# Kernel optimization log

Measured on AMD Instinct MI355X. Metric: run time of the kernel, lower is better.

The kernel has to match this reference:

```python
import jax, jax.numpy as jnp
import numpy as np

B, N, E, H = 4, 2048, 288, 8
D = E // H  # head_dim = 36


def setup_inputs() -> dict:
    key = jax.random.key(0)
    ks = jax.random.split(key, 8)
    s = 1.0 / np.sqrt(E)
    return {
        "query": jax.random.normal(ks[0], (B, N, E), jnp.float32),
        "key": jax.random.normal(ks[1], (B, N, E), jnp.float32),
        "value": jax.random.normal(ks[2], (B, N, E), jnp.float32),
        "Wq": jax.random.normal(ks[3], (E, E), jnp.float32) * s,
        "bq": jnp.zeros((E,), jnp.float32),
        "Wk": jax.random.normal(ks[4], (E, E), jnp.float32) * s,
        "bk": jnp.zeros((E,), jnp.float32),
        "Wv": jax.random.normal(ks[5], (E, E), jnp.float32) * s,
        "bv": jnp.zeros((E,), jnp.float32),
        "Wo": jax.random.normal(ks[6], (E, E), jnp.float32) * s,
        "bo": jnp.zeros((E,), jnp.float32),
    }


def reference(query, key, value, Wq, bq, Wk, bk, Wv, bv, Wo, bo):
    scaling = float(D) ** (-0.5)
    q = (query @ Wq + bq) * scaling            # (B, N, E), pre-scaled as in source
    k = key @ Wk + bk                          # (B, N, E)
    v = value @ Wv + bv                        # (B, N, E)
    # split heads: per-head slices along last dim == reshape to (B, N, H, D)
    qh = q.reshape(B, N, H, D)
    kh = k.reshape(B, N, H, D)
    vh = v.reshape(B, N, H, D)
    scores = jnp.einsum("bnhd,bmhd->bhnm", qh, kh)   # (B, H, N, N)
    attn = jax.nn.softmax(scores, axis=-1)
    out = jnp.einsum("bhnm,bmhd->bnhd", attn, vh)    # (B, N, H, D)
    out = out.reshape(B, N, E)                       # concat heads
    return out @ Wo + bo
```

## Files before the change

kernel.cpp:

```cpp
#include <hip/hip_runtime.h>

#define E 288
#define NSEQ 2048
#define BATCH 4
#define NH 8
#define HD 36
#define BH (BATCH * NH)
#define ROWS (BATCH * NSEQ)
#define BHN (BH * NSEQ)

typedef _Float16 half8_t __attribute__((ext_vector_type(8)));
typedef _Float16 half4_t __attribute__((ext_vector_type(4)));
typedef float f32x4 __attribute__((ext_vector_type(4)));
typedef int i32x4 __attribute__((ext_vector_type(4)));

__device__ __forceinline__ int sw64(int row, int col) {
  return (row << 6) + ((((col >> 3) ^ row) & 7) << 3) + (col & 7);
}

__device__ __forceinline__ int toff(int r, int k) {
  const int rp = r >> 1;
  const int g = (((r & 1) << 2) + (k >> 3)) ^ (rp & 7);
  return (rp << 6) + ((g & 7) << 3) + (k & 7);
}

__device__ __forceinline__ void gld16(const _Float16* g, _Float16* l) {
  __builtin_amdgcn_global_load_lds(
      (const __attribute__((address_space(1))) void*)g,
      (__attribute__((address_space(3))) void*)l, 16, 0, 0);
}

__device__ __forceinline__ float fexp2(float x) {
  return __builtin_amdgcn_exp2f(x);
}

#define WBLK 1296
#define QZBLK 2048

__global__ __launch_bounds__(256) void prep_kernel(
    const float* __restrict__ Wq, const float* __restrict__ Wk,
    const float* __restrict__ Wv, const float* __restrict__ Wo,
    _Float16* __restrict__ wblk, _Float16* __restrict__ q16) {
  const int bid = blockIdx.x;
  const int tid = threadIdx.x;
  if (bid < WBLK) {
    const int j = bid * 256 + tid;
    const int m = j / (E * E);
    const int rem = j - m * (E * E);
    const int k = rem / E, n = rem - k * E;
    const float* W = (m == 0) ? Wq : (m == 1) ? Wk : (m == 2) ? Wv : Wo;
    wblk[(size_t)((m * 3 + n / 96) * 9 + (k >> 5)) * 3072 +
         toff(n % 96, k & 31)] = (_Float16)W[(size_t)k * E + n];
  } else {
    const int j = (bid - WBLK) * 256 + tid;
    ((i32x4*)q16)[j] = (i32x4){0, 0, 0, 0};
  }
}

#define PM 128
#define PN 96

struct QKVArgs {
  const float* x[3];
  const float* bias[3];
  _Float16* out[3];
};

__global__ __launch_bounds__(256, 4) void proj_qkv_kernel(
    QKVArgs A, const _Float16* __restrict__ wblk) {
  __shared__ __align__(16) _Float16 abuf[2][4096];
  __shared__ __align__(16) _Float16 wbuf[2][3072];

  const int tid = threadIdx.x;
  const int lane = tid & 63, w = tid >> 6;
  const int quad = lane >> 4, l15 = lane & 15;
  const int mode = blockIdx.z;
  const int RB = blockIdx.x, CT = blockIdx.y;
  const float* __restrict__ x = A.x[mode];
  const _Float16* __restrict__ wb = wblk + (size_t)(mode * 3 + CT) * 9 * 3072;
  const int row0 = RB * PM;

  float4 apre[4];
  auto loadA = [&](int C) {
#pragma unroll
    for (int iu = 0; iu < 4; ++iu) {
      const int i = tid + 256 * iu, r = i >> 3, c4 = i & 7;
      apre[iu] = *(const float4*)&x[(size_t)(row0 + r) * E + C * 32 + c4 * 4];
    }
  };
  auto writeA = [&](_Float16* dst) {
#pragma unroll
    for (int iu = 0; iu < 4; ++iu) {
      const int i = tid + 256 * iu, r = i >> 3, c4 = i & 7;
      half4_t h = {(_Float16)apre[iu].x, (_Float16)apre[iu].y,
                   (_Float16)apre[iu].z, (_Float16)apre[iu].w};
      *(half4_t*)&dst[toff(r, c4 * 4)] = h;
    }
  };

  f32x4 acc[2][6];
#pragma unroll
  for (int t = 0; t < 2; ++t)
#pragma unroll
    for (int nt = 0; nt < 6; ++nt) acc[t][nt] = (f32x4){0.f, 0.f, 0.f, 0.f};

  loadA(0);
  writeA(abuf[0]);
  for (int seg = w; seg < 6; seg += 4)
    gld16(wb + seg * 512 + lane * 8, wbuf[0] + seg * 512);
  loadA(1);

  for (int C = 0; C < 9; ++C) {
    const int cur = C & 1;
    __syncthreads();
    if (C + 1 < 9) {
      for (int seg = w; seg < 6; seg += 4)
        gld16(wb + (C + 1) * 3072 + seg * 512 + lane * 8,
              wbuf[cur ^ 1] + seg * 512);
      writeA(abuf[cur ^ 1]);
      if (C + 2 < 9) loadA(C + 2);
    }
    half8_t ah[2];
#pragma unroll
    for (int t = 0; t < 2; ++t)
      ah[t] = *(const half8_t*)&abuf[cur][toff(w * 32 + t * 16 + l15, quad * 8)];
#pragma unroll
    for (int nt = 0; nt < 6; ++nt) {
      const half8_t bf = *(const half8_t*)&wbuf[cur][toff(nt * 16 + l15, quad * 8)];
#pragma unroll
      for (int t = 0; t < 2; ++t)
        acc[t][nt] = __builtin_amdgcn_mfma_f32_16x16x32_f16(ah[t], bf, acc[t][nt], 0, 0, 0);
    }
  }

  const float* __restrict__ bias = A.bias[mode];
  _Float16* __restrict__ outp = A.out[mode];
  const float scale = (mode == 0) ? 0.24044917348149868f : 1.0f;
  const int col0 = CT * PN;
#pragma unroll
  for (int nt = 0; nt < 6; ++nt) {
    const int col = col0 + nt * 16 + l15;
    const int h = col / 36, d = col - h * 36;
    const float bc = bias[col];
#pragma unroll
    for (int t = 0; t < 2; ++t) {
#pragma unroll
      for (int r = 0; r < 4; ++r) {
        const int row = row0 + w * 32 + t * 16 + quad * 4 + r;
        const int b = row >> 11, n = row & (NSEQ - 1);
        const int bh = b * NH + h;
        const _Float16 val = (_Float16)((acc[t][nt][r] + bc) * scale);
        if (mode == 0) {
          outp[((size_t)bh * NSEQ + n) * 64 + d] = val;
        } else {
          const int kt = n >> 6, c = n & 63;
          if (mode == 1) {
            outp[((size_t)bh * 32 + kt) * 4096 + sw64(c, d)] = val;
          } else {
            const int pc = ((c & 15) << 2) | (c >> 4);
            outp[((size_t)bh * 32 + kt) * 3072 + sw64(d, pc)] = val;
          }
        }
      }
    }
  }
}

#define QB 128
#define KT 64
#define SPLIT 4

__device__ __forceinline__ void stage_tile(const _Float16* kg, const _Float16* vg,
                                           _Float16* kb, _Float16* vb, int w,
                                           int lane) {
#pragma unroll
  for (int seg = w; seg < 8; seg += 4)
    gld16(kg + seg * 512 + lane * 8, kb + seg * 512);
  for (int seg = w; seg < 6; seg += 4)
    gld16(vg + seg * 512 + lane * 8, vb + seg * 512);
}

__global__ __launch_bounds__(256, 4) void attn_kernel(
    const _Float16* __restrict__ q16, const _Float16* __restrict__ kblk,
    const _Float16* __restrict__ vblk, _Float16* __restrict__ pacc16,
    float* __restrict__ psum) {
  __shared__ __align__(16) _Float16 kbuf[2][KT * 64];
  __shared__ __align__(16) _Float16 vbuf[2][48 * 64];
  __shared__ __align__(16) _Float16 pbuf[4][16 * 64];

  const int tid = threadIdx.x;
  const int lane = tid & 63;
  const int w = tid >> 6;
  const int quad = lane >> 4;
  const int l15 = lane & 15;

  const int id = blockIdx.x;
  const int xcd = id & 7;
  const int qb = (id >> 3) & 15;
  const int g = id >> 7;
  const int bhc = g * 8 + xcd;
  const int bh = bhc >> 2;
  const int chunk = bhc & 3;
  const int q0 = qb * QB;

  const _Float16* qbase = q16 + ((size_t)bh * NSEQ + q0 + w * 32) * 64;
  half8_t qf[2][2];
#pragma unroll
  for (int t = 0; t < 2; ++t)
#pragma unroll
    for (int kc = 0; kc < 2; ++kc)
      qf[t][kc] = *(const half8_t*)&qbase[(t * 16 + l15) * 64 + kc * 32 + quad * 8];

  f32x4 oacc[2][3];
#pragma unroll
  for (int t = 0; t < 2; ++t)
#pragma unroll
    for (int nt = 0; nt < 3; ++nt) oacc[t][nt] = (f32x4){0.f, 0.f, 0.f, 0.f};
  float ssum[2][4] = {{0.f, 0.f, 0.f, 0.f}, {0.f, 0.f, 0.f, 0.f}};

  const int t0 = chunk * 8;
  const _Float16* kbase = kblk + ((size_t)bh * 32 + t0) * 4096;
  const _Float16* vbase = vblk + ((size_t)bh * 32 + t0) * 3072;

  stage_tile(kbase, vbase, kbuf[0], vbuf[0], w, lane);

  for (int it = 0; it < 8; ++it) {
    const int cur = it & 1;
    __syncthreads();
    if (it + 1 < 8)
      stage_tile(kbase + (it + 1) * 4096, vbase + (it + 1) * 3072,
                 kbuf[cur ^ 1], vbuf[cur ^ 1], w, lane);

    half8_t vf[2][3];
#pragma unroll
    for (int kc = 0; kc < 2; ++kc)
#pragma unroll
      for (int nt = 0; nt < 3; ++nt)
        vf[kc][nt] = *(const half8_t*)&vbuf[cur][sw64(nt * 16 + l15, kc * 32 + quad * 8)];

#pragma unroll
    for (int t = 0; t < 2; ++t) {
      f32x4 sc[4];
#pragma unroll
      for (int s = 0; s < 4; ++s) {
        const half8_t kf0 = *(const half8_t*)&kbuf[cur][sw64(s * 16 + l15, quad * 8)];
        const half8_t kf1 = *(const half8_t*)&kbuf[cur][sw64(s * 16 + l15, 32 + quad * 8)];
        f32x4 c0 = __builtin_amdgcn_mfma_f32_16x16x32_f16(
            qf[t][0], kf0, (f32x4){0.f, 0.f, 0.f, 0.f}, 0, 0, 0);
        sc[s] = __builtin_amdgcn_mfma_f32_16x16x32_f16(qf[t][1], kf1, c0, 0, 0, 0);
      }
#pragma unroll
      for (int r = 0; r < 4; ++r) {
        const float p0 = fexp2(sc[0][r]);
        const float p1 = fexp2(sc[1][r]);
        const float p2 = fexp2(sc[2][r]);
        const float p3 = fexp2(sc[3][r]);
        ssum[t][r] += (p0 + p1) + (p2 + p3);
        half4_t ph = {(_Float16)p0, (_Float16)p1, (_Float16)p2, (_Float16)p3};
        *(half4_t*)&pbuf[w][sw64(quad * 4 + r, l15 * 4)] = ph;
      }
#pragma unroll
      for (int kc = 0; kc < 2; ++kc) {
        const half8_t af = *(const half8_t*)&pbuf[w][sw64(l15, kc * 32 + quad * 8)];
#pragma unroll
        for (int nt = 0; nt < 3; ++nt)
          oacc[t][nt] = __builtin_amdgcn_mfma_f32_16x16x32_f16(af, vf[kc][nt], oacc[t][nt], 0, 0, 0);
      }
    }
  }

#pragma unroll
  for (int t = 0; t < 2; ++t) {
#pragma unroll
    for (int r = 0; r < 4; ++r) {
      float s = ssum[t][r];
      s += __shfl_xor(s, 1);
      s += __shfl_xor(s, 2);
      s += __shfl_xor(s, 4);
      s += __shfl_xor(s, 8);
      const int row = q0 + w * 32 + t * 16 + quad * 4 + r;
      const size_t gr = (size_t)chunk * BHN + (size_t)bh * NSEQ + row;
      if (l15 == 0) psum[gr] = s;
#pragma unroll
      for (int nt = 0; nt < 3; ++nt) {
        const int col = nt * 16 + l15;
        if (col < HD) pacc16[gr * HD + col] = (_Float16)oacc[t][nt][r];
      }
    }
  }
}

__global__ __launch_bounds__(256) void combine_kernel(
    const _Float16* __restrict__ pacc16, const float* __restrict__ psum,
    _Float16* __restrict__ abh, _Float16* __restrict__ abl) {
  const int idx = blockIdx.x * 256 + threadIdx.x;
  if (idx >= BHN * 9) return;
  const int gr = idx / 9;
  const int d4 = idx - gr * 9;

  float a[4] = {0.f, 0.f, 0.f, 0.f};
  float s = 0.f;
#pragma unroll
  for (int c = 0; c < SPLIT; ++c) {
    const half4_t p = *(const half4_t*)&pacc16[((size_t)c * BHN + gr) * HD + d4 * 4];
#pragma unroll
    for (int j = 0; j < 4; ++j) a[j] += (float)p[j];
    s += psum[(size_t)c * BHN + gr];
  }
  const float inv = 1.0f / s;
  const int bh = gr >> 11;
  const int n = gr & (NSEQ - 1);
  const int b = bh >> 3, h = bh & 7;
  const int row = b * NSEQ + n;
  const int col = h * 36 + d4 * 4;

  half4_t hv, lv;
#pragma unroll
  for (int j = 0; j < 4; ++j) {
    const float val = a[j] * inv;
    const _Float16 hi = (_Float16)val;
    hv[j] = hi;
    lv[j] = (_Float16)(val - (float)hi);
  }
  const size_t o = (size_t)((row >> 6) * 9 + (col >> 5)) * 2048 + toff(row & 63, col & 31);
  *(half4_t*)&abh[o] = hv;
  *(half4_t*)&abl[o] = lv;
}

__global__ __launch_bounds__(256, 4) void proj_o_kernel(
    const _Float16* __restrict__ abh, const _Float16* __restrict__ abl,
    const _Float16* __restrict__ wblk_o, const float* __restrict__ bias,
    float* __restrict__ out) {
  __shared__ __align__(16) _Float16 hbuf[2][2048];
  __shared__ __align__(16) _Float16 lbuf[2][2048];
  __shared__ __align__(16) _Float16 wbuf[2][3072];

  const int tid = threadIdx.x;
  const int lane = tid & 63, w = tid >> 6;
  const int quad = lane >> 4, l15 = lane & 15;
  const int RB = blockIdx.x, CT = blockIdx.y;
  const _Float16* __restrict__ hblk = abh + (size_t)RB * 9 * 2048;
  const _Float16* __restrict__ lblk = abl + (size_t)RB * 9 * 2048;
  const _Float16* __restrict__ wb = wblk_o + (size_t)CT * 9 * 3072;

  f32x4 acc[6];
#pragma unroll
  for (int nt = 0; nt < 6; ++nt) acc[nt] = (f32x4){0.f, 0.f, 0.f, 0.f};

  gld16(hblk + w * 512 + lane * 8, hbuf[0] + w * 512);
  gld16(lblk + w * 512 + lane * 8, lbuf[0] + w * 512);
  for (int seg = w; seg < 6; seg += 4)
    gld16(wb + seg * 512 + lane * 8, wbuf[0] + seg * 512);

  for (int C = 0; C < 9; ++C) {
    const int cur = C & 1;
    __syncthreads();
    if (C + 1 < 9) {
      gld16(hblk + (C + 1) * 2048 + w * 512 + lane * 8, hbuf[cur ^ 1] + w * 512);
      gld16(lblk + (C + 1) * 2048 + w * 512 + lane * 8, lbuf[cur ^ 1] + w * 512);
      for (int seg = w; seg < 6; seg += 4)
        gld16(wb + (C + 1) * 3072 + seg * 512 + lane * 8, wbuf[cur ^ 1] + seg * 512);
    }
    const half8_t ah = *(const half8_t*)&hbuf[cur][toff(w * 16 + l15, quad * 8)];
    const half8_t al = *(const half8_t*)&lbuf[cur][toff(w * 16 + l15, quad * 8)];
#pragma unroll
    for (int nt = 0; nt < 6; ++nt) {
      const half8_t bf = *(const half8_t*)&wbuf[cur][toff(nt * 16 + l15, quad * 8)];
      acc[nt] = __builtin_amdgcn_mfma_f32_16x16x32_f16(ah, bf, acc[nt], 0, 0, 0);
      acc[nt] = __builtin_amdgcn_mfma_f32_16x16x32_f16(al, bf, acc[nt], 0, 0, 0);
    }
  }

#pragma unroll
  for (int nt = 0; nt < 6; ++nt) {
    const int col = CT * PN + nt * 16 + l15;
    const float bc = bias[col];
#pragma unroll
    for (int r = 0; r < 4; ++r) {
      const int row = RB * 64 + w * 16 + quad * 4 + r;
      out[(size_t)row * E + col] = acc[nt][r] + bc;
    }
  }
}

extern "C" void kernel_launch(void* const* d_in, const int* in_sizes, int n_in,
                              void* d_out, int out_size, void* d_ws,
                              size_t ws_size, hipStream_t stream) {
  const float* query = (const float*)d_in[0];
  const float* key_ = (const float*)d_in[1];
  const float* value = (const float*)d_in[2];
  const float* Wq = (const float*)d_in[3];
  const float* bq = (const float*)d_in[4];
  const float* Wk = (const float*)d_in[5];
  const float* bk = (const float*)d_in[6];
  const float* Wv = (const float*)d_in[7];
  const float* bv = (const float*)d_in[8];
  const float* Wo = (const float*)d_in[9];
  const float* bo = (const float*)d_in[10];
  float* out = (float*)d_out;

  _Float16* q16 = (_Float16*)d_ws;
  _Float16* kblk = q16 + (size_t)BH * NSEQ * 64;
  _Float16* vblk = kblk + (size_t)BH * 32 * 4096;
  _Float16* wblk = vblk + (size_t)BH * 32 * 3072;
  _Float16* abh = wblk + (size_t)4 * 3 * 9 * 3072;
  _Float16* abl = abh + (size_t)128 * 9 * 2048;
  _Float16* pacc16 = abl + (size_t)128 * 9 * 2048;
  float* psum = (float*)(pacc16 + (size_t)SPLIT * BHN * HD);

  prep_kernel<<<WBLK + QZBLK, 256, 0, stream>>>(Wq, Wk, Wv, Wo, wblk, q16);

  QKVArgs qa;
  qa.x[0] = query; qa.x[1] = key_; qa.x[2] = value;
  qa.bias[0] = bq; qa.bias[1] = bk; qa.bias[2] = bv;
  qa.out[0] = q16; qa.out[1] = kblk; qa.out[2] = vblk;
  proj_qkv_kernel<<<dim3(ROWS / PM, E / PN, 3), 256, 0, stream>>>(qa, wblk);

  attn_kernel<<<dim3((NSEQ / QB) * BH * SPLIT), 256, 0, stream>>>(
      q16, kblk, vblk, pacc16, psum);

  combine_kernel<<<(BHN * 9) / 256, 256, 0, stream>>>(pacc16, psum, abh, abl);

  proj_o_kernel<<<dim3(ROWS / 64, E / PN), 256, 0, stream>>>(
      abh, abl, wblk + (size_t)3 * 3 * 9 * 3072, bo, out);
}
```

Before: 165.8 us.

## Transpose QK^T MFMA and redistribute P via permlane swaps instead of LDS

Swaps the MFMA operands so scores come out as S^T, which puts each query row in a lane. The fp16 probabilities are then reshaped into the A-operand layout for the PV MFMA using v_permlane16/32_swap in registers, which removes the per-wave pbuf LDS write/read round trip. Row sums become a per-lane accumulation plus two cross-lane shuffles instead of four. The risk is that the permlane register layout is subtle and could be wrong, and the PV loop now reloads V fragments from LDS inside the loop.

```diff
diff --git a/kernel.cpp b/kernel.cpp
--- a/kernel.cpp
+++ b/kernel.cpp
@@ -11,6 +11,7 @@
 
 typedef _Float16 half8_t __attribute__((ext_vector_type(8)));
 typedef _Float16 half4_t __attribute__((ext_vector_type(4)));
+typedef _Float16 half2_t __attribute__((ext_vector_type(2)));
 typedef float f32x4 __attribute__((ext_vector_type(4)));
 typedef int i32x4 __attribute__((ext_vector_type(4)));
 
@@ -32,6 +33,20 @@
 
 __device__ __forceinline__ float fexp2(float x) {
   return __builtin_amdgcn_exp2f(x);
+}
+
+__device__ __forceinline__ unsigned pack_h2(float a, float b) {
+  union { half2_t h; unsigned u; } cv;
+  cv.h[0] = (_Float16)a;
+  cv.h[1] = (_Float16)b;
+  return cv.u;
+}
+
+__device__ __forceinline__ void plswap16(unsigned& a, unsigned& b) {
+  asm("v_permlane16_swap_b32 %0, %1" : "+v"(a), "+v"(b));
+}
+__device__ __forceinline__ void plswap32(unsigned& a, unsigned& b) {
+  asm("v_permlane32_swap_b32 %0, %1" : "+v"(a), "+v"(b));
 }
 
 #define WBLK 1296
@@ -186,7 +201,6 @@
     float* __restrict__ psum) {
   __shared__ __align__(16) _Float16 kbuf[2][KT * 64];
   __shared__ __align__(16) _Float16 vbuf[2][48 * 64];
-  __shared__ __align__(16) _Float16 pbuf[4][16 * 64];
 
   const int tid = threadIdx.x;
   const int lane = tid & 63;
@@ -216,7 +230,7 @@
   for (int t = 0; t < 2; ++t)
 #pragma unroll
     for (int nt = 0; nt < 3; ++nt) oacc[t][nt] = (f32x4){0.f, 0.f, 0.f, 0.f};
-  float ssum[2][4] = {{0.f, 0.f, 0.f, 0.f}, {0.f, 0.f, 0.f, 0.f}};
+  float ssum[2] = {0.f, 0.f};
 
   const int t0 = chunk * 8;
   const _Float16* kbase = kblk + ((size_t)bh * 32 + t0) * 4096;
@@ -231,56 +245,74 @@
       stage_tile(kbase + (it + 1) * 4096, vbase + (it + 1) * 3072,
                  kbuf[cur ^ 1], vbuf[cur ^ 1], w, lane);
 
-    half8_t vf[2][3];
-#pragma unroll
-    for (int kc = 0; kc < 2; ++kc)
-#pragma unroll
-      for (int nt = 0; nt < 3; ++nt)
-        vf[kc][nt] = *(const half8_t*)&vbuf[cur][sw64(nt * 16 + l15, kc * 32 + quad * 8)];
-
-#pragma unroll
-    for (int t = 0; t < 2; ++t) {
-      f32x4 sc[4];
-#pragma unroll
-      for (int s = 0; s < 4; ++s) {
+    unsigned pk[2][4][2];
+#pragma unroll
+    for (int a = 0; a < 2; ++a) {
+      f32x4 sc[2][2];
+#pragma unroll
+      for (int sp = 0; sp < 2; ++sp) {
+        const int s = a * 2 + sp;
         const half8_t kf0 = *(const half8_t*)&kbuf[cur][sw64(s * 16 + l15, quad * 8)];
         const half8_t kf1 = *(const half8_t*)&kbuf[cur][sw64(s * 16 + l15, 32 + quad * 8)];
-        f32x4 c0 = __builtin_amdgcn_mfma_f32_16x16x32_f16(
-            qf[t][0], kf0, (f32x4){0.f, 0.f, 0.f, 0.f}, 0, 0, 0);
-        sc[s] = __builtin_amdgcn_mfma_f32_16x16x32_f16(qf[t][1], kf1, c0, 0, 0, 0);
+#pragma unroll
+        for (int t = 0; t < 2; ++t) {
+          f32x4 c0 = __builtin_amdgcn_mfma_f32_16x16x32_f16(
+              kf0, qf[t][0], (f32x4){0.f, 0.f, 0.f, 0.f}, 0, 0, 0);
+          sc[t][sp] = __builtin_amdgcn_mfma_f32_16x16x32_f16(
+              kf1, qf[t][1], c0, 0, 0, 0);
+        }
       }
 #pragma unroll
-      for (int r = 0; r < 4; ++r) {
-        const float p0 = fexp2(sc[0][r]);
-        const float p1 = fexp2(sc[1][r]);
-        const float p2 = fexp2(sc[2][r]);
-        const float p3 = fexp2(sc[3][r]);
-        ssum[t][r] += (p0 + p1) + (p2 + p3);
-        half4_t ph = {(_Float16)p0, (_Float16)p1, (_Float16)p2, (_Float16)p3};
-        *(half4_t*)&pbuf[w][sw64(quad * 4 + r, l15 * 4)] = ph;
+      for (int t = 0; t < 2; ++t)
+#pragma unroll
+        for (int r = 0; r < 4; ++r) {
+          const float p0 = fexp2(sc[t][0][r]);
+          const float p1 = fexp2(sc[t][1][r]);
+          ssum[t] += p0 + p1;
+          pk[t][r][a] = pack_h2(p0, p1);
+        }
+    }
+
+    half8_t pa[2][2];
+#pragma unroll
+    for (int t = 0; t < 2; ++t) {
+      union { unsigned u[4]; half8_t h; } f0, f1;
+#pragma unroll
+      for (int v = 0; v < 4; ++v) {
+        unsigned x = pk[t][v >> 1][v & 1];
+        unsigned y = pk[t][(v >> 1) + 2][v & 1];
+        plswap16(x, y);
+        plswap32(x, y);
+        f0.u[v] = x;
+        f1.u[v] = y;
       }
-#pragma unroll
-      for (int kc = 0; kc < 2; ++kc) {
-        const half8_t af = *(const half8_t*)&pbuf[w][sw64(l15, kc * 32 + quad * 8)];
-#pragma unroll
-        for (int nt = 0; nt < 3; ++nt)
-          oacc[t][nt] = __builtin_amdgcn_mfma_f32_16x16x32_f16(af, vf[kc][nt], oacc[t][nt], 0, 0, 0);
+      pa[t][0] = f0.h;
+      pa[t][1] = f1.h;
+    }
+
+#pragma unroll
+    for (int kc = 0; kc < 2; ++kc)
+#pragma unroll
+      for (int nt = 0; nt < 3; ++nt) {
+        const half8_t vf = *(const half8_t*)&vbuf[cur][sw64(nt * 16 + l15, kc * 32 + quad * 8)];
+#pragma unroll
+        for (int t = 0; t < 2; ++t)
+          oacc[t][nt] = __builtin_amdgcn_mfma_f32_16x16x32_f16(pa[t][kc], vf, oacc[t][nt], 0, 0, 0);
       }
-    }
   }
 
 #pragma unroll
   for (int t = 0; t < 2; ++t) {
+    float s = ssum[t];
+    s += __shfl_xor(s, 16);
+    s += __shfl_xor(s, 32);
+    const int rowq = q0 + w * 32 + t * 16 + l15;
+    const size_t grq = (size_t)chunk * BHN + (size_t)bh * NSEQ + rowq;
+    if (lane < 16) psum[grq] = s;
 #pragma unroll
     for (int r = 0; r < 4; ++r) {
-      float s = ssum[t][r];
-      s += __shfl_xor(s, 1);
-      s += __shfl_xor(s, 2);
-      s += __shfl_xor(s, 4);
-      s += __shfl_xor(s, 8);
       const int row = q0 + w * 32 + t * 16 + quad * 4 + r;
       const size_t gr = (size_t)chunk * BHN + (size_t)bh * NSEQ + row;
-      if (l15 == 0) psum[gr] = s;
 #pragma unroll
       for (int nt = 0; nt < 3; ++nt) {
         const int col = nt * 16 + l15;
```

Result: faster. 162.2 us (-2.2%).
